# Kernel tuning notes

Measured on AMD Instinct MI355X. Metric: run time of the kernel, lower is better.

## Reference

```python
import jax, jax.numpy as jnp
import numpy as np

B, S, D, H, DFF = 4, 2048, 1024, 16, 4096
DK = D // H
EPS = 1e-9


def setup_inputs() -> dict:
    key = jax.random.key(0)
    ks = jax.random.split(key, 12)
    s = lambda k, shape, scale: jax.random.normal(k, shape, dtype=jnp.float32) * scale
    return {
        "x": s(ks[0], (B, S, D), 1.0),
        "mask": jnp.ones((B, 1, 1, S), dtype=jnp.int32),
        # Linear weights stored torch-style [out, in]
        "wq": s(ks[1], (D, D), D ** -0.5),
        "wk": s(ks[2], (D, D), D ** -0.5),
        "wv": s(ks[3], (D, D), D ** -0.5),
        "wo": s(ks[4], (D, D), D ** -0.5),
        "w1": s(ks[5], (DFF, D), D ** -0.5),
        "b1": jnp.zeros((DFF,), jnp.float32),
        "w2": s(ks[6], (D, DFF), DFF ** -0.5),
        "b2": jnp.zeros((D,), jnp.float32),
        "g1": jnp.ones((D,), jnp.float32),
        "be1": jnp.zeros((D,), jnp.float32),
        "g2": jnp.ones((D,), jnp.float32),
        "be2": jnp.zeros((D,), jnp.float32),
    }


def _layernorm(x, gamma, beta):
    # Matches AddAndNorm: torch.std uses Bessel correction (ddof=1)
    mean = jnp.mean(x, axis=-1, keepdims=True)
    var = jnp.sum((x - mean) ** 2, axis=-1, keepdims=True) / (x.shape[-1] - 1)
    return gamma * (x - mean) / jnp.sqrt(var + EPS) + beta


def _mha(x, mask, wq, wk, wv, wo):
    b, s, d = x.shape
    def proj(w):  # [b,s,d] @ [d,d]^T -> heads [b,h,s,dk]
        return (x @ w.T).reshape(b, s, H, DK).transpose(0, 2, 1, 3)
    q, k, v = proj(wq), proj(wk), proj(wv)
    scores = jnp.einsum("bhqd,bhkd->bhqk", q, k) / jnp.sqrt(jnp.float32(DK))
    scores = jnp.where(mask == 0, jnp.float32(-1e9), scores)
    attn = jax.nn.softmax(scores, axis=-1)
    out = jnp.einsum("bhqk,bhkd->bhqd", attn, v)
    out = out.transpose(0, 2, 1, 3).reshape(b, s, d)
    return out @ wo.T


def reference(x, mask, wq, wk, wv, wo, w1, b1, w2, b2, g1, be1, g2, be2):
    # Residual 1: x + MHA(LN(x))  (dropout = 0)
    h1 = x + _mha(_layernorm(x, g1, be1), mask, wq, wk, wv, wo)
    # Residual 2: h1 + FFN(LN(h1))
    z = _layernorm(h1, g2, be2)
    ffn = jax.nn.relu(z @ w1.T + b1) @ w2.T + b2
    return h1 + ffn
```

## Files before the change

### kernel.cpp

```cpp
#include <hip/hip_runtime.h>
#include <hip/hip_bf16.h>
#include <cstdint>
#include <cstddef>

typedef __attribute__((ext_vector_type(8))) short short8;
typedef __attribute__((ext_vector_type(4))) float floatx4;
typedef __attribute__((ext_vector_type(4))) unsigned short ushort4e;

#define B_   4
#define S_   2048
#define D_   1024
#define H_   16
#define DK_  64
#define DFF_ 4096
#define MTOT (B_ * S_)
#define QKVLD 3072

__device__ __forceinline__ float bf2f(unsigned short u) {
    union { unsigned int i; float f; } v; v.i = ((unsigned int)u) << 16; return v.f;
}
__device__ __forceinline__ unsigned short f2bf(float f) {
    union { float f; unsigned int i; } v; v.f = f;
    unsigned int u = v.i;
    u += 0x7fffu + ((u >> 16) & 1u);
    return (unsigned short)(u >> 16);
}
__device__ __forceinline__ void async_cp16(const void* g, void* l) {
    __builtin_amdgcn_global_load_lds(
        (const __attribute__((address_space(1))) unsigned int*)g,
        (__attribute__((address_space(3))) unsigned int*)l,
        16, 0, 0);
}

__global__ void dtype_probe(const unsigned short* __restrict__ x, int* flag) {
    __shared__ float red[4];
    const int tid = threadIdx.x;
    float mx = 0.f;
    #pragma unroll
    for (int i = 0; i < 16; i++) {
        float v = fabsf(bf2f(x[tid * 16 + i]));
        if (v != v) v = 1e30f;
        mx = fmaxf(mx, v);
    }
    #pragma unroll
    for (int off = 32; off > 0; off >>= 1) mx = fmaxf(mx, __shfl_down(mx, off));
    if ((tid & 63) == 0) red[tid >> 6] = mx;
    __syncthreads();
    if (tid == 0) {
        float m = fmaxf(fmaxf(red[0], red[1]), fmaxf(red[2], red[3]));
        *flag = (m > 50.f) ? 1 : 0;
    }
}

__device__ __forceinline__ void cvt8(const void* src, unsigned short* dst, int i, int fl) {
    if (fl) {
        const floatx4* s = (const floatx4*)src;
        floatx4 a = s[i * 2], b = s[i * 2 + 1];
        short8 o;
        o[0] = (short)f2bf(a[0]); o[1] = (short)f2bf(a[1]);
        o[2] = (short)f2bf(a[2]); o[3] = (short)f2bf(a[3]);
        o[4] = (short)f2bf(b[0]); o[5] = (short)f2bf(b[1]);
        o[6] = (short)f2bf(b[2]); o[7] = (short)f2bf(b[3]);
        ((short8*)dst)[i] = o;
    } else {
        ((short8*)dst)[i] = ((const short8*)src)[i];
    }
}

__global__ void cvt_kernel(const void* __restrict__ src,
                           unsigned short* __restrict__ dst,
                           int n8, const int* __restrict__ flag) {
    const int i = blockIdx.x * 256 + threadIdx.x;
    if (i >= n8) return;
    cvt8(src, dst, i, *flag);
}

__global__ void cvt4_kernel(const void* s0, const void* s1, const void* s2, const void* s3,
                            unsigned short* __restrict__ dst,
                            const int* __restrict__ flag) {
    const int t = blockIdx.x >> 9;
    const int i = (blockIdx.x & 511) * 256 + threadIdx.x;
    const void* s = (t == 0) ? s0 : (t == 1) ? s1 : (t == 2) ? s2 : s3;
    cvt8(s, dst + (size_t)t * (D_ * D_), i, *flag);
}

__global__ void cvt_small(const void* b1, const void* b2, const void* g1,
                          const void* be1, const void* g2, const void* be2,
                          unsigned short* db1, unsigned short* db2, unsigned short* dg1,
                          unsigned short* dbe1, unsigned short* dg2, unsigned short* dbe2,
                          const int* __restrict__ flag) {
    const int fl = *flag;
    for (int i = threadIdx.x; i < 1152; i += 256) {
        if (i < 512)       cvt8(b1,  db1,  i,        fl);
        else if (i < 640)  cvt8(b2,  db2,  i - 512,  fl);
        else if (i < 768)  cvt8(g1,  dg1,  i - 640,  fl);
        else if (i < 896)  cvt8(be1, dbe1, i - 768,  fl);
        else if (i < 1024) cvt8(g2,  dg2,  i - 896,  fl);
        else               cvt8(be2, dbe2, i - 1024, fl);
    }
}

#define BM 128
#define BN 128
#define BK 64

template<int RELU, int HAS_BIAS, int RES_MODE, int OUT_MODE>
__global__ __launch_bounds__(256)
void gemm_bt(const unsigned short* __restrict__ A, int lda,
             const unsigned short* __restrict__ W, int ldw,
             const unsigned short* __restrict__ bias,
             const void* resid,
             void* out,
             int M, int N, int K,
             const int* __restrict__ flagp)
{
    __shared__ unsigned short As[BM * BK];
    __shared__ unsigned short Bs[BN * BK];

    const int tid  = threadIdx.x;
    const int lane = tid & 63;
    const int wave = tid >> 6;
    const int wm = wave >> 1;
    const int wn = wave & 1;
    const int lr = lane & 15;
    const int lq = lane >> 4;

    const int m0 = blockIdx.y * BM;
    const int n0 = blockIdx.x * BN;

    int fl = 1;
    if (RES_MODE == 3 || OUT_MODE == 2) fl = *flagp;

    floatx4 acc[4][4];
    #pragma unroll
    for (int i = 0; i < 4; i++)
        #pragma unroll
        for (int j = 0; j < 4; j++)
            acc[i][j] = (floatx4){0.f, 0.f, 0.f, 0.f};

    const int lrow = lane >> 3;
    const int swz  = ((lane & 7) ^ lrow) * 8;
    const int rx   = lr & 7;
    const int p0   = ((lq)     ^ rx) * 8;
    const int p1   = ((4 + lq) ^ rx) * 8;

    for (int k0 = 0; k0 < K; k0 += BK) {
        #pragma unroll
        for (int t = 0; t < 4; t++) {
            const int row = wave * 32 + t * 8;
            async_cp16(A + (size_t)(m0 + row + lrow) * lda + k0 + swz, &As[row * BK]);
            async_cp16(W + (size_t)(n0 + row + lrow) * ldw + k0 + swz, &Bs[row * BK]);
        }
        __syncthreads();
        #pragma unroll
        for (int kk = 0; kk < 2; kk++) {
            const int pos = kk ? p1 : p0;
            short8 af[4], bfr[4];
            #pragma unroll
            for (int i = 0; i < 4; i++) {
                af[i]  = *(const short8*)(&As[(wm * 64 + i * 16 + lr) * BK + pos]);
                bfr[i] = *(const short8*)(&Bs[(wn * 64 + i * 16 + lr) * BK + pos]);
            }
            #pragma unroll
            for (int i = 0; i < 4; i++)
                #pragma unroll
                for (int j = 0; j < 4; j++)
                    acc[i][j] = __builtin_amdgcn_mfma_f32_16x16x32_bf16(
                                    af[i], bfr[j], acc[i][j], 0, 0, 0);
        }
        __syncthreads();
    }

    #pragma unroll
    for (int i = 0; i < 4; i++) {
        #pragma unroll
        for (int j = 0; j < 4; j++) {
            const int col = n0 + wn * 64 + j * 16 + lr;
            const float bv = HAS_BIAS ? bf2f(bias[col]) : 0.f;
            #pragma unroll
            for (int r = 0; r < 4; r++) {
                const int row = m0 + wm * 64 + i * 16 + lq * 4 + r;
                const size_t idx = (size_t)row * N + col;
                float vvv = acc[i][j][r] + bv;
                if (RES_MODE == 1) vvv += bf2f(((const unsigned short*)resid)[idx]);
                if (RES_MODE == 2) vvv += ((const float*)resid)[idx];
                if (RES_MODE == 3) vvv += fl ? ((const float*)resid)[idx]
                                             : bf2f(((const unsigned short*)resid)[idx]);
                if (RELU) vvv = fmaxf(vvv, 0.f);
                if (OUT_MODE == 1)      ((float*)out)[idx] = vvv;
                else if (OUT_MODE == 0) ((unsigned short*)out)[idx] = f2bf(vvv);
                else { if (fl) ((float*)out)[idx] = vvv;
                       else    ((unsigned short*)out)[idx] = f2bf(vvv); }
            }
        }
    }
}

template<int IN_MODE>
__global__ __launch_bounds__(256)
void ln_kernel(const void* __restrict__ Xv,
               const unsigned short* __restrict__ g,
               const unsigned short* __restrict__ be,
               unsigned short* __restrict__ out,
               const int* __restrict__ flagp)
{
    const int row = blockIdx.x;
    const int tid = threadIdx.x;
    int fl = 1;
    if (IN_MODE == 2) fl = *flagp;
    float x4[4];
    if (IN_MODE == 1 || fl) {
        const float* X = (const float*)Xv + (size_t)row * D_ + tid * 4;
        floatx4 t = *(const floatx4*)X;
        x4[0] = t[0]; x4[1] = t[1]; x4[2] = t[2]; x4[3] = t[3];
    } else {
        const unsigned short* X = (const unsigned short*)Xv + (size_t)row * D_ + tid * 4;
        ushort4e u = *(const ushort4e*)X;
        #pragma unroll
        for (int i = 0; i < 4; i++) x4[i] = bf2f(u[i]);
    }
    float s1 = x4[0] + x4[1] + x4[2] + x4[3];
    float s2 = x4[0]*x4[0] + x4[1]*x4[1] + x4[2]*x4[2] + x4[3]*x4[3];
    #pragma unroll
    for (int off = 32; off > 0; off >>= 1) {
        s1 += __shfl_down(s1, off);
        s2 += __shfl_down(s2, off);
    }
    __shared__ float r1[4], r2[4];
    const int wv = tid >> 6;
    if ((tid & 63) == 0) { r1[wv] = s1; r2[wv] = s2; }
    __syncthreads();
    s1 = r1[0] + r1[1] + r1[2] + r1[3];
    s2 = r2[0] + r2[1] + r2[2] + r2[3];
    const float mean = s1 * (1.0f / D_);
    const float var  = (s2 - (float)D_ * mean * mean) * (1.0f / (D_ - 1));
    const float rstd = rsqrtf(var + 1e-9f);

    ushort4e o4;
    #pragma unroll
    for (int i = 0; i < 4; i++) {
        const float gv = bf2f(g[tid * 4 + i]);
        const float bv = bf2f(be[tid * 4 + i]);
        o4[i] = f2bf(gv * (x4[i] - mean) * rstd + bv);
    }
    *(ushort4e*)(out + (size_t)row * D_ + tid * 4) = o4;
}

__global__ __launch_bounds__(256)
void vtrans(const unsigned short* __restrict__ V, int ldv,
            unsigned short* __restrict__ Vt)
{
    __shared__ unsigned short t[64 * 72];
    const int tid = threadIdx.x;
    const int kt  = blockIdx.x * 64;
    const int bh  = blockIdx.y;
    const int b   = bh >> 4, h = bh & 15;
    const int r   = tid >> 2;
    const int c4  = (tid & 3) * 16;
    const unsigned short* vp = V + (size_t)(b * S_ + kt + r) * ldv + h * DK_ + c4;
    *(short8*)&t[r * 72 + c4]     = *(const short8*)vp;
    *(short8*)&t[r * 72 + c4 + 8] = *(const short8*)(vp + 8);
    __syncthreads();
    short8 o0, o1;
    #pragma unroll
    for (int e = 0; e < 8; e++) {
        o0[e] = (short)t[(c4 + e) * 72 + r];
        o1[e] = (short)t[(c4 + 8 + e) * 72 + r];
    }
    unsigned short* op = Vt + ((size_t)bh * DK_ + r) * S_ + kt + c4;
    *(short8*)op       = o0;
    *(short8*)(op + 8) = o1;
}

#define ATK   64
#define KS_LD 64
#define PS_LD 72
#define NT_   (S_ / ATK)

__global__ __launch_bounds__(256)
void attn_mfma(const unsigned short* __restrict__ QKV,
               const unsigned short* __restrict__ Vt,
               const int* __restrict__ mask,
               unsigned short* __restrict__ ctx)
{
    __shared__ unsigned short Ks[ATK * KS_LD];
    __shared__ unsigned short Vts[DK_ * KS_LD];
    __shared__ unsigned short Ps[4][32 * PS_LD];
    __shared__ float maskadd[ATK];
    __shared__ float ared[4][32];

    const int tid  = threadIdx.x;
    const int lane = tid & 63;
    const int w    = tid >> 6;
    const int c    = lane & 15;
    const int qd   = lane >> 4;

    const int flat    = blockIdx.y * gridDim.x + blockIdx.x;
    const int logical = (flat & 7) * 128 + (flat >> 3);
    const int bh   = logical >> 4;
    const int b    = bh >> 4;
    const int h    = bh & 15;
    const int q0   = (logical & 15) * 128 + w * 32;

    const int lrow = lane >> 3;
    const int swz  = ((lane & 7) ^ lrow) * 8;
    const int cx   = c & 7;

    const float QS = 0.18033688f;
    short8 qf[2][2];
    #pragma unroll
    for (int jq = 0; jq < 2; jq++)
        #pragma unroll
        for (int kk = 0; kk < 2; kk++) {
            const unsigned short* qp =
                QKV + (size_t)(b * S_ + q0 + jq * 16 + c) * QKVLD + h * DK_ + kk * 32 + qd * 8;
            short8 t = *(const short8*)qp;
            short8 o;
            #pragma unroll
            for (int e = 0; e < 8; e++)
                o[e] = (short)f2bf(bf2f((unsigned short)t[e]) * QS);
            qf[jq][kk] = o;
        }

    floatx4 acc_o[2][4];
    #pragma unroll
    for (int iq = 0; iq < 2; iq++)
        #pragma unroll
        for (int jd = 0; jd < 4; jd++)
            acc_o[iq][jd] = (floatx4){0.f, 0.f, 0.f, 0.f};
    float lrun[2] = {0.f, 0.f};

    for (int kt = 0; kt < S_; kt += ATK) {
        {
            const unsigned short* kbase =
                QKV + 1024 + (size_t)(b * S_ + kt + w * 16) * QKVLD + h * DK_;
            const unsigned short* vbase =
                Vt + ((size_t)bh * DK_ + w * 16) * S_ + kt;
            #pragma unroll
            for (int t = 0; t < 2; t++) {
                async_cp16(kbase + (size_t)(t * 8 + lrow) * QKVLD + swz,
                           &Ks[(w * 16 + t * 8) * KS_LD]);
                async_cp16(vbase + (size_t)(t * 8 + lrow) * S_ + swz,
                           &Vts[(w * 16 + t * 8) * KS_LD]);
            }
            if (tid < ATK) maskadd[tid] = (mask[b * S_ + kt + tid] == 0) ? -1e9f : 0.f;
        }
        __syncthreads();

        floatx4 acc_s[4][2];
        #pragma unroll
        for (int i = 0; i < 4; i++)
            #pragma unroll
            for (int jq = 0; jq < 2; jq++)
                acc_s[i][jq] = (floatx4){0.f, 0.f, 0.f, 0.f};
        #pragma unroll
        for (int kk = 0; kk < 2; kk++) {
            const int pos = ((kk * 4 + qd) ^ cx) * 8;
            short8 kf[4];
            #pragma unroll
            for (int i = 0; i < 4; i++)
                kf[i] = *(const short8*)&Ks[(i * 16 + c) * KS_LD + pos];
            __builtin_amdgcn_s_setprio(1);
            #pragma unroll
            for (int i = 0; i < 4; i++)
                #pragma unroll
                for (int jq = 0; jq < 2; jq++)
                    acc_s[i][jq] = __builtin_amdgcn_mfma_f32_16x16x32_bf16(
                                       kf[i], qf[jq][kk], acc_s[i][jq], 0, 0, 0);
            __builtin_amdgcn_s_setprio(0);
        }

        floatx4 madd[4];
        #pragma unroll
        for (int i = 0; i < 4; i++)
            madd[i] = *(const floatx4*)&maskadd[i * 16 + qd * 4];

        #pragma unroll
        for (int jq = 0; jq < 2; jq++) {
            float ps = 0.f;
            #pragma unroll
            for (int i = 0; i < 4; i++) {
                floatx4 p;
                #pragma unroll
                for (int r = 0; r < 4; r++) {
                    p[r] = __builtin_amdgcn_exp2f(acc_s[i][jq][r] + madd[i][r]);
                    ps += p[r];
                }
                unsigned int w0, w1;
                asm("v_cvt_pk_bf16_f32 %0, %1, %2" : "=v"(w0) : "v"(p[0]), "v"(p[1]));
                asm("v_cvt_pk_bf16_f32 %0, %1, %2" : "=v"(w1) : "v"(p[2]), "v"(p[3]));
                uint2 pk; pk.x = w0; pk.y = w1;
                *(uint2*)&Ps[w][(jq * 16 + c) * PS_LD + i * 16 + qd * 4] = pk;
            }
            ps += __shfl_xor(ps, 16);
            ps += __shfl_xor(ps, 32);
            lrun[jq] += ps;
        }

        #pragma unroll
        for (int kk = 0; kk < 2; kk++) {
            const int pos = ((kk * 4 + qd) ^ cx) * 8;
            short8 pf[2], vf[4];
            #pragma unroll
            for (int iq = 0; iq < 2; iq++)
                pf[iq] = *(const short8*)&Ps[w][(iq * 16 + c) * PS_LD + kk * 32 + qd * 8];
            #pragma unroll
            for (int jd = 0; jd < 4; jd++)
                vf[jd] = *(const short8*)&Vts[(jd * 16 + c) * KS_LD + pos];
            __builtin_amdgcn_s_setprio(1);
            #pragma unroll
            for (int iq = 0; iq < 2; iq++)
                #pragma unroll
                for (int jd = 0; jd < 4; jd++)
                    acc_o[iq][jd] = __builtin_amdgcn_mfma_f32_16x16x32_bf16(
                                        pf[iq], vf[jd], acc_o[iq][jd], 0, 0, 0);
            __builtin_amdgcn_s_setprio(0);
        }
        __syncthreads();
    }

    if (lane < 16) { ared[w][c] = 1.f / lrun[0]; ared[w][16 + c] = 1.f / lrun[1]; }
    floatx4 lv0 = *(const floatx4*)&ared[w][qd * 4];
    floatx4 lv1 = *(const floatx4*)&ared[w][16 + qd * 4];
    #pragma unroll
    for (int iq = 0; iq < 2; iq++)
        #pragma unroll
        for (int jd = 0; jd < 4; jd++)
            #pragma unroll
            for (int r = 0; r < 4; r++) {
                const int row = q0 + iq * 16 + qd * 4 + r;
                const int col = h * DK_ + jd * 16 + c;
                const float inv = (iq == 0) ? lv0[r] : lv1[r];
                ctx[(size_t)(b * S_ + row) * D_ + col] = f2bf(acc_o[iq][jd][r] * inv);
            }
}

extern "C" void kernel_launch(void* const* d_in, const int* in_sizes, int n_in,
                              void* d_out, int out_size, void* d_ws, size_t ws_size,
                              hipStream_t stream)
{
    const void* x_raw  = d_in[0];
    const int*  mask   = (const int*)d_in[1];
    const void* wq_raw = d_in[2];
    const void* wk_raw = d_in[3];
    const void* wv_raw = d_in[4];
    const void* wo_raw = d_in[5];
    const void* w1_raw = d_in[6];
    const void* b1_raw = d_in[7];
    const void* w2_raw = d_in[8];
    const void* b2_raw = d_in[9];
    const void* g1_raw = d_in[10];
    const void* be1_raw= d_in[11];
    const void* g2_raw = d_in[12];
    const void* be2_raw= d_in[13];

    char* ws = (char*)d_ws;
    const size_t MB = 1024 * 1024;
    int* flag = (int*)ws;
    unsigned short* cb1  = (unsigned short*)(ws + 1 * 1024);
    unsigned short* cb2  = (unsigned short*)(ws + 16 * 1024);
    unsigned short* cg1  = (unsigned short*)(ws + 32 * 1024);
    unsigned short* cbe1 = (unsigned short*)(ws + 40 * 1024);
    unsigned short* cg2  = (unsigned short*)(ws + 48 * 1024);
    unsigned short* cbe2 = (unsigned short*)(ws + 56 * 1024);
    unsigned short* cwqkvo = (unsigned short*)(ws + 1 * MB);
    unsigned short* cwqkv  = cwqkvo;
    unsigned short* cwo    = cwqkvo + 3 * (D_ * D_);
    unsigned short* cw1  = (unsigned short*)(ws + 9 * MB);
    unsigned short* cw2  = (unsigned short*)(ws + 17 * MB);
    unsigned short* xn1  = (unsigned short*)(ws + 25 * MB);
    unsigned short* ctx  = (unsigned short*)(ws + 25 * MB);
    unsigned short* zbuf = (unsigned short*)(ws + 25 * MB);
    unsigned short* qkv  = (unsigned short*)(ws + 41 * MB);
    float*          h1   = (float*)(ws + 57 * MB);
    unsigned short* vt   = (unsigned short*)d_out;
    unsigned short* xn2  = (unsigned short*)d_out;

    dtype_probe<<<1, 256, 0, stream>>>((const unsigned short*)x_raw, flag);
    cvt_small<<<1, 256, 0, stream>>>(b1_raw, b2_raw, g1_raw, be1_raw, g2_raw, be2_raw,
                                     cb1, cb2, cg1, cbe1, cg2, cbe2, flag);
    cvt4_kernel<<<2048, 256, 0, stream>>>(wq_raw, wk_raw, wv_raw, wo_raw, cwqkvo, flag);
    cvt_kernel<<<(DFF_ * D_ / 8 + 255) / 256, 256, 0, stream>>>(w1_raw, cw1, DFF_ * D_ / 8, flag);
    cvt_kernel<<<(D_ * DFF_ / 8 + 255) / 256, 256, 0, stream>>>(w2_raw, cw2, D_ * DFF_ / 8, flag);

    const dim3 blk(256);
    const dim3 gs(D_ / BN, MTOT / BM);
    const dim3 gsq(QKVLD / BN, MTOT / BM);
    const dim3 gs2(2048 / BN, MTOT / BM);

    ln_kernel<2><<<MTOT, blk, 0, stream>>>(x_raw, cg1, cbe1, xn1, flag);
    gemm_bt<0,0,0,0><<<gsq, blk, 0, stream>>>(xn1, D_, cwqkv, D_, nullptr, nullptr, qkv, MTOT, QKVLD, D_, flag);
    vtrans<<<dim3(S_ / 64, B_ * H_), blk, 0, stream>>>(qkv + 2048, QKVLD, vt);
    attn_mfma<<<dim3(S_ / 128, B_ * H_), blk, 0, stream>>>(qkv, vt, mask, ctx);
    gemm_bt<0,0,3,1><<<gs, blk, 0, stream>>>(ctx, D_, cwo, D_, nullptr, x_raw, h1, MTOT, D_, D_, flag);
    ln_kernel<1><<<MTOT, blk, 0, stream>>>(h1, cg2, cbe2, xn2, flag);
    gemm_bt<1,1,0,0><<<gs2, blk, 0, stream>>>(xn2, D_, cw1, D_, cb1, nullptr, zbuf, MTOT, 2048, D_, flag);
    gemm_bt<0,0,2,1><<<gs, blk, 0, stream>>>(zbuf, 2048, cw2, DFF_, nullptr, h1, h1, MTOT, D_, 2048, flag);
    const unsigned short* w1c = cw1 + (size_t)2048 * D_;
    gemm_bt<1,1,0,0><<<gs2, blk, 0, stream>>>(xn2, D_, w1c, D_, cb1 + 2048, nullptr, zbuf, MTOT, 2048, D_, flag);
    gemm_bt<0,1,2,2><<<gs, blk, 0, stream>>>(zbuf, 2048, cw2 + 2048, DFF_, cb2, h1, d_out, MTOT, D_, 2048, flag);
}
```

Measured before the change: 578.8 us.

## Add 256x256-tile double-buffered GEMM kernel for QKV and FFN1 projections

Adds a new 512-thread GEMM kernel with 256x256 output tiles, 64-wide K steps, double-buffered LDS filled by async copies interleaved with MFMA phases, and s_setprio around the MFMA bursts. It replaces the existing 128-tile GEMM for the QKV projection and both FFN-up halves, which have K=1024 and large N. Larger tiles raise arithmetic intensity per global load. In exchange it uses 128 KB of LDS per block and many accumulator registers, which limits occupancy, and it yields fewer blocks per grid (e.g. 12x32 for QKV).

Result: no change. 569.6 us (-1.6%).

```diff
diff --git a/kernel.cpp b/kernel.cpp
--- a/kernel.cpp
+++ b/kernel.cpp
@@ -191,6 +191,132 @@
                 else if (OUT_MODE == 0) ((unsigned short*)out)[idx] = f2bf(vvv);
                 else { if (fl) ((float*)out)[idx] = vvv;
                        else    ((unsigned short*)out)[idx] = f2bf(vvv); }
+            }
+        }
+    }
+}
+
+#define GBM 256
+#define GBN 256
+#define GBK 64
+
+__device__ __forceinline__ void gbar() {
+    asm volatile("" ::: "memory");
+    __builtin_amdgcn_s_barrier();
+    asm volatile("" ::: "memory");
+}
+
+template<int RELU, int HAS_BIAS>
+__global__ __launch_bounds__(512, 2)
+void gemm256_bt(const unsigned short* __restrict__ A, int lda,
+                const unsigned short* __restrict__ W, int ldw,
+                const unsigned short* __restrict__ bias,
+                unsigned short* __restrict__ out,
+                int M, int N, int K)
+{
+    __shared__ unsigned short As[2][GBM * GBK];
+    __shared__ unsigned short Bs[2][GBN * GBK];
+
+    const int tid  = threadIdx.x;
+    const int lane = tid & 63;
+    const int wave = tid >> 6;
+    const int wm   = wave >> 2;
+    const int wn   = wave & 3;
+    const int lr   = lane & 15;
+    const int lq   = lane >> 4;
+
+    const int m0 = blockIdx.y * GBM;
+    const int n0 = blockIdx.x * GBN;
+
+    const int lrow = lane >> 3;
+    const int schk = ((lane & 7) ^ lrow) * 8;
+    const int rx   = lr & 7;
+    const int fp0  = ((lq)     ^ rx) * 8;
+    const int fp1  = ((4 + lq) ^ rx) * 8;
+
+    floatx4 acc[8][4];
+    #pragma unroll
+    for (int i = 0; i < 8; i++)
+        #pragma unroll
+        for (int j = 0; j < 4; j++)
+            acc[i][j] = (floatx4){0.f, 0.f, 0.f, 0.f};
+
+    const int nkt = K / GBK;
+
+    #pragma unroll
+    for (int g = 0; g < 4; g++) {
+        async_cp16(A + (size_t)(m0 + g * 64 + wave * 8 + lrow) * lda + schk,
+                   &As[0][g * 4096 + wave * 512]);
+        async_cp16(W + (size_t)(n0 + g * 64 + wave * 8 + lrow) * ldw + schk,
+                   &Bs[0][g * 4096 + wave * 512]);
+    }
+    asm volatile("s_waitcnt vmcnt(0)" ::: "memory");
+    __syncthreads();
+
+    for (int t = 0; t < nkt; ++t) {
+        const int cur   = t & 1;
+        const int knext = (t + 1) * GBK;
+        const bool more = (t + 1 < nkt);
+        short8 bfr[4][2];
+
+        #pragma unroll
+        for (int p = 0; p < 4; ++p) {
+            short8 af[2][2];
+            #pragma unroll
+            for (int ii = 0; ii < 2; ii++)
+                #pragma unroll
+                for (int kk = 0; kk < 2; kk++)
+                    af[ii][kk] = *(const short8*)
+                        &As[cur][(wm * 128 + p * 32 + ii * 16 + lr) * GBK + (kk ? fp1 : fp0)];
+            if (p == 0) {
+                #pragma unroll
+                for (int j = 0; j < 4; j++)
+                    #pragma unroll
+                    for (int kk = 0; kk < 2; kk++)
+                        bfr[j][kk] = *(const short8*)
+                            &Bs[cur][(wn * 64 + j * 16 + lr) * GBK + (kk ? fp1 : fp0)];
+                if (more) {
+                    #pragma unroll
+                    for (int g = 0; g < 4; g++)
+                        async_cp16(A + (size_t)(m0 + g * 64 + wave * 8 + lrow) * lda + knext + schk,
+                                   &As[cur ^ 1][g * 4096 + wave * 512]);
+                }
+            }
+            if (p == 1 && more) {
+                #pragma unroll
+                for (int g = 0; g < 4; g++)
+                    async_cp16(W + (size_t)(n0 + g * 64 + wave * 8 + lrow) * ldw + knext + schk,
+                               &Bs[cur ^ 1][g * 4096 + wave * 512]);
+            }
+            if (p == 3) asm volatile("s_waitcnt vmcnt(0)" ::: "memory");
+            gbar();
+            __builtin_amdgcn_s_setprio(1);
+            #pragma unroll
+            for (int kk = 0; kk < 2; kk++)
+                #pragma unroll
+                for (int ii = 0; ii < 2; ii++)
+                    #pragma unroll
+                    for (int j = 0; j < 4; j++)
+                        acc[p * 2 + ii][j] = __builtin_amdgcn_mfma_f32_16x16x32_bf16(
+                                                 af[ii][kk], bfr[j][kk],
+                                                 acc[p * 2 + ii][j], 0, 0, 0);
+            __builtin_amdgcn_s_setprio(0);
+            gbar();
+        }
+    }
+
+    #pragma unroll
+    for (int i = 0; i < 8; i++) {
+        #pragma unroll
+        for (int j = 0; j < 4; j++) {
+            const int col = n0 + wn * 64 + j * 16 + lr;
+            const float bv = HAS_BIAS ? bf2f(bias[col]) : 0.f;
+            #pragma unroll
+            for (int r = 0; r < 4; r++) {
+                const int row = m0 + wm * 128 + i * 16 + lq * 4 + r;
+                float vvv = acc[i][j][r] + bv;
+                if (RELU) vvv = fmaxf(vvv, 0.f);
+                out[(size_t)row * N + col] = f2bf(vvv);
             }
         }
     }
@@ -484,19 +610,20 @@
     cvt_kernel<<<(D_ * DFF_ / 8 + 255) / 256, 256, 0, stream>>>(w2_raw, cw2, D_ * DFF_ / 8, flag);
 
     const dim3 blk(256);
+    const dim3 blk5(512);
     const dim3 gs(D_ / BN, MTOT / BM);
-    const dim3 gsq(QKVLD / BN, MTOT / BM);
-    const dim3 gs2(2048 / BN, MTOT / BM);
+    const dim3 gq256(QKVLD / GBN, MTOT / GBM);
+    const dim3 gf256(2048 / GBN, MTOT / GBM);
 
     ln_kernel<2><<<MTOT, blk, 0, stream>>>(x_raw, cg1, cbe1, xn1, flag);
-    gemm_bt<0,0,0,0><<<gsq, blk, 0, stream>>>(xn1, D_, cwqkv, D_, nullptr, nullptr, qkv, MTOT, QKVLD, D_, flag);
+    gemm256_bt<0,0><<<gq256, blk5, 0, stream>>>(xn1, D_, cwqkv, D_, nullptr, qkv, MTOT, QKVLD, D_);
     vtrans<<<dim3(S_ / 64, B_ * H_), blk, 0, stream>>>(qkv + 2048, QKVLD, vt);
     attn_mfma<<<dim3(S_ / 128, B_ * H_), blk, 0, stream>>>(qkv, vt, mask, ctx);
     gemm_bt<0,0,3,1><<<gs, blk, 0, stream>>>(ctx, D_, cwo, D_, nullptr, x_raw, h1, MTOT, D_, D_, flag);
     ln_kernel<1><<<MTOT, blk, 0, stream>>>(h1, cg2, cbe2, xn2, flag);
-    gemm_bt<1,1,0,0><<<gs2, blk, 0, stream>>>(xn2, D_, cw1, D_, cb1, nullptr, zbuf, MTOT, 2048, D_, flag);
+    gemm256_bt<1,1><<<gf256, blk5, 0, stream>>>(xn2, D_, cw1, D_, cb1, zbuf, MTOT, 2048, D_);
     gemm_bt<0,0,2,1><<<gs, blk, 0, stream>>>(zbuf, 2048, cw2, DFF_, nullptr, h1, h1, MTOT, D_, 2048, flag);
     const unsigned short* w1c = cw1 + (size_t)2048 * D_;
-    gemm_bt<1,1,0,0><<<gs2, blk, 0, stream>>>(xn2, D_, w1c, D_, cb1 + 2048, nullptr, zbuf, MTOT, 2048, D_, flag);
+    gemm256_bt<1,1><<<gf256, blk5, 0, stream>>>(xn2, D_, w1c, D_, cb1 + 2048, zbuf, MTOT, 2048, D_);
     gemm_bt<0,1,2,2><<<gs, blk, 0, stream>>>(zbuf, 2048, cw2 + 2048, DFF_, cb2, h1, d_out, MTOT, D_, 2048, flag);
 }
```
